# Optimization experiments

Measured on AMD Instinct MI355X. Metric: run time of the kernel, lower is better.

## Reference

```python
import jax, jax.numpy as jnp
import numpy as np

N = 50000      # nodes
E = 800000     # edges (before self-loops)
D_IN = 256     # input feature dim
H = 4          # attention heads
C = 32         # per-head channels
HID = H * C    # 128, concat output dim
BN_EPS = 1e-5


def setup_inputs() -> dict:
    key = jax.random.key(0)
    ks = jax.random.split(key, 24)
    inp = {}
    inp["x"] = jax.random.normal(ks[0], (N, D_IN), jnp.float32)
    inp["edge_index"] = jax.random.randint(ks[1], (2, E), 0, N, jnp.int32)
    # layer 1 GATConv params
    inp["W1"] = jax.random.normal(ks[2], (D_IN, HID), jnp.float32) * (2.0 / (D_IN + HID)) ** 0.5
    inp["att_src1"] = jax.random.normal(ks[3], (H, C), jnp.float32) * 0.1
    inp["att_dst1"] = jax.random.normal(ks[4], (H, C), jnp.float32) * 0.1
    inp["bias1"] = jnp.zeros((HID,), jnp.float32)
    # layer 1 BatchNorm (eval mode)
    inp["gamma1"] = 1.0 + 0.1 * jax.random.normal(ks[5], (HID,), jnp.float32)
    inp["beta1"] = 0.1 * jax.random.normal(ks[6], (HID,), jnp.float32)
    inp["mean1"] = 0.1 * jax.random.normal(ks[7], (HID,), jnp.float32)
    inp["var1"] = 0.5 + jax.random.uniform(ks[8], (HID,), jnp.float32)
    # layer 2 GATConv params
    inp["W2"] = jax.random.normal(ks[9], (HID, HID), jnp.float32) * (2.0 / (HID + HID)) ** 0.5
    inp["att_src2"] = jax.random.normal(ks[10], (H, C), jnp.float32) * 0.1
    inp["att_dst2"] = jax.random.normal(ks[11], (H, C), jnp.float32) * 0.1
    inp["bias2"] = jnp.zeros((HID,), jnp.float32)
    # layer 2 BatchNorm (eval mode)
    inp["gamma2"] = 1.0 + 0.1 * jax.random.normal(ks[12], (HID,), jnp.float32)
    inp["beta2"] = 0.1 * jax.random.normal(ks[13], (HID,), jnp.float32)
    inp["mean2"] = 0.1 * jax.random.normal(ks[14], (HID,), jnp.float32)
    inp["var2"] = 0.5 + jax.random.uniform(ks[15], (HID,), jnp.float32)
    return inp


def _gat_layer(x, src, dst, W, att_src, att_dst, bias):
    # x: [N, D]; src/dst: [Etot] with self-loops already appended
    h = (x @ W).reshape(N, H, C)                       # [N, H, C]
    a_s = jnp.einsum("nhc,hc->nh", h, att_src)         # [N, H]
    a_d = jnp.einsum("nhc,hc->nh", h, att_dst)         # [N, H]
    e = jax.nn.leaky_relu(a_s[src] + a_d[dst], 0.2)    # [Etot, H]
    # edge softmax over incoming edges of each destination node
    m = jax.ops.segment_max(e, dst, num_segments=N)    # [N, H]
    ex = jnp.exp(e - m[dst])                           # [Etot, H]
    den = jax.ops.segment_sum(ex, dst, num_segments=N) # [N, H]
    alpha = ex / (den[dst] + 1e-16)                    # [Etot, H]
    out = jax.ops.segment_sum(h[src] * alpha[:, :, None], dst, num_segments=N)
    return out.reshape(N, HID) + bias                  # concat heads + bias


def _bn_eval(x, gamma, beta, mean, var):
    return (x - mean) * (gamma * jax.lax.rsqrt(var + BN_EPS)) + beta


def reference(x, edge_index, W1, att_src1, att_dst1, bias1, gamma1, beta1, mean1, var1,
              W2, att_src2, att_dst2, bias2, gamma2, beta2, mean2, var2):
    loop = jnp.arange(N, dtype=edge_index.dtype)
    src = jnp.concatenate([edge_index[0], loop])  # PyG GATConv adds self-loops
    dst = jnp.concatenate([edge_index[1], loop])
    h = _gat_layer(x, src, dst, W1, att_src1, att_dst1, bias1)
    h = jax.nn.relu(_bn_eval(h, gamma1, beta1, mean1, var1))  # dropout = identity (eval)
    h = _gat_layer(h, src, dst, W2, att_src2, att_dst2, bias2)
    h = jax.nn.relu(_bn_eval(h, gamma2, beta2, mean2, var2))
    return h
```

## Files before the change

### kernel.cpp

```cpp
#include <hip/hip_runtime.h>
#include <math.h>

#define N_NODES 50000
#define EDGES   800000
#define ETOT    (EDGES + N_NODES)
#define HID     128
#define NH      4

typedef __attribute__((ext_vector_type(8))) short short8;
typedef __attribute__((ext_vector_type(4))) float floatx4;

__device__ inline unsigned short f2bf(float f) {
    unsigned int u = __float_as_uint(f);
    u = u + 0x7FFFu + ((u >> 16) & 1u);
    return (unsigned short)(u >> 16);
}

#define NB 391
#define BCAP 2688
#define CHUNK 4096
#define BIN_BLOCKS ((ETOT + CHUNK - 1) / CHUNK)

__global__ __launch_bounds__(256) void init_cursor_kernel(int* __restrict__ cursor) {
    int t = blockIdx.x * 256 + threadIdx.x;
    if (t < NB) cursor[t] = t * BCAP;
}

__global__ __launch_bounds__(256) void bin_scatter_kernel(const int* __restrict__ ei,
                                                          int* __restrict__ cursor,
                                                          int* __restrict__ binned) {
    __shared__ int histL[NB];
    int t = threadIdx.x;
    for (int b = t; b < NB; b += 256) histL[b] = 0;
    __syncthreads();
    int base = blockIdx.x * CHUNK;
#pragma unroll
    for (int j = 0; j < 16; j++) {
        int e = base + j * 256 + t;
        if (e < ETOT) {
            int d = (e < EDGES) ? ei[EDGES + e] : (e - EDGES);
            atomicAdd(&histL[d >> 7], 1);
        }
    }
    __syncthreads();
    for (int b = t; b < NB; b += 256) {
        int c = histL[b];
        histL[b] = c ? atomicAdd(&cursor[b], c) : 0;
    }
    __syncthreads();
#pragma unroll
    for (int j = 0; j < 16; j++) {
        int e = base + j * 256 + t;
        if (e < ETOT) {
            int s, d;
            if (e < EDGES) { s = ei[e]; d = ei[EDGES + e]; }
            else           { s = d = e - EDGES; }
            int bb = d >> 7;
            int pos = atomicAdd(&histL[bb], 1);
            if (pos < (bb + 1) * BCAP)
                binned[pos] = (s << 7) | (d & 127);
        }
    }
}

__global__ __launch_bounds__(256) void bin_finalize_kernel(const int* __restrict__ binned,
                                                           const int* __restrict__ cursor,
                                                           int* __restrict__ starts,
                                                           int* __restrict__ degs,
                                                           int* __restrict__ csr) {
    __shared__ int histN[128];
    __shared__ int excl[128];
    int b = blockIdx.x, t = threadIdx.x;
    int n0 = b << 7;
    int S = b * BCAP;
    int cnt = cursor[b] - S;
    if (cnt > BCAP) cnt = BCAP;
    if (t < 128) histN[t] = 0;
    __syncthreads();
    for (int j = t; j < cnt; j += 256)
        atomicAdd(&histN[binned[S + j] & 127], 1);
    __syncthreads();
    int v = (t < 128) ? histN[t] : 0;
    if (t < 128) excl[t] = v;
    __syncthreads();
    for (int off = 1; off < 128; off <<= 1) {
        int x = 0, add = 0;
        if (t < 128) { x = excl[t]; if (t >= off) add = excl[t - off]; }
        __syncthreads();
        if (t < 128) excl[t] = x + add;
        __syncthreads();
    }
    if (t < 128) {
        int ex = excl[t] - v;
        int n = n0 + t;
        if (n < N_NODES) { starts[n] = S + ex; degs[n] = v; }
        histN[t] = ex;
    }
    __syncthreads();
    for (int j = t; j < cnt; j += 256) {
        int e = binned[S + j];
        int pos = atomicAdd(&histN[e & 127], 1);
        csr[S + pos] = e >> 7;
    }
}

__global__ void wtrans_coef_kernel(const float* __restrict__ W1, const float* __restrict__ W2,
                                   unsigned short* __restrict__ Wt1, unsigned short* __restrict__ Wt2,
                                   const float* __restrict__ b1, const float* __restrict__ g1,
                                   const float* __restrict__ be1, const float* __restrict__ mn1,
                                   const float* __restrict__ vr1,
                                   const float* __restrict__ b2, const float* __restrict__ g2,
                                   const float* __restrict__ be2, const float* __restrict__ mn2,
                                   const float* __restrict__ vr2, float* __restrict__ coef) {
    int i = blockIdx.x * 256 + threadIdx.x;
    if (i < 256 * 128) { int k = i >> 7, n = i & 127; Wt1[n * 256 + k] = f2bf(W1[i]); }
    if (i < 128 * 128) { int k = i >> 7, n = i & 127; Wt2[n * 128 + k] = f2bf(W2[i]); }
    if (blockIdx.x == 0) {
        int t = threadIdx.x;
        if (t < 128) {
            float sc = g1[t] * rsqrtf(vr1[t] + 1e-5f);
            coef[t]       = sc;
            coef[128 + t] = be1[t] + (b1[t] - mn1[t]) * sc;
        } else {
            int c = t - 128;
            float sc = g2[c] * rsqrtf(vr2[c] + 1e-5f);
            coef[256 + c] = sc;
            coef[384 + c] = be2[c] + (b2[c] - mn2[c]) * sc;
        }
    }
}

#define GR   64
#define KC   64
#define PADK 88
#define PADH 136

union Smem {
    struct { unsigned short Xs[GR][PADK]; unsigned short Ws[HID][PADK]; } s;
    unsigned short Hs[GR][PADH];
};

template<bool XBF16>
__global__ __launch_bounds__(256) void gemm_att_kernel(const void* __restrict__ Xv,
                                                       const unsigned short* __restrict__ Wt,
                                                       const float* __restrict__ att_src,
                                                       const float* __restrict__ att_dst,
                                                       unsigned short* __restrict__ Hout,
                                                       float* __restrict__ aS,
                                                       float* __restrict__ aD, int K) {
    __shared__ Smem sm;
    int t = threadIdx.x, lane = t & 63, w = t >> 6;
    int quad = lane >> 4, nl = lane & 15;
    int rowBase = blockIdx.x * GR;

    floatx4 acc[8];
    floatx4 zero = {0.f, 0.f, 0.f, 0.f};
#pragma unroll
    for (int b = 0; b < 8; b++) acc[b] = zero;

    const float*          Xf = (const float*)Xv;
    const unsigned short* Xb = (const unsigned short*)Xv;

    for (int k0 = 0; k0 < K; k0 += KC) {
#pragma unroll
        for (int it = 0; it < 2; it++) {
            int s5 = t + it * 256;
            int row = s5 >> 3, kg = s5 & 7;
            int gr = rowBase + row;
            unsigned short tmp[8];
            if (XBF16) {
                uint4 v = make_uint4(0, 0, 0, 0);
                if (gr < N_NODES) v = *(const uint4*)&Xb[(unsigned)(gr * K + k0 + kg * 8)];
                *(uint4*)tmp = v;
            } else {
                float4 v0 = make_float4(0, 0, 0, 0), v1 = v0;
                if (gr < N_NODES) {
                    const float* p = &Xf[(unsigned)(gr * K + k0 + kg * 8)];
                    v0 = *(const float4*)p;
                    v1 = *(const float4*)(p + 4);
                }
                tmp[0] = f2bf(v0.x); tmp[1] = f2bf(v0.y); tmp[2] = f2bf(v0.z); tmp[3] = f2bf(v0.w);
                tmp[4] = f2bf(v1.x); tmp[5] = f2bf(v1.y); tmp[6] = f2bf(v1.z); tmp[7] = f2bf(v1.w);
            }
            *(uint4*)&sm.s.Xs[row][kg * 8] = *(uint4*)tmp;
        }
#pragma unroll
        for (int it = 0; it < 4; it++) {
            int s5 = t + it * 256;
            int n = s5 >> 3, kg = s5 & 7;
            *(uint4*)&sm.s.Ws[n][kg * 8] = *(const uint4*)&Wt[(unsigned)(n * K + k0 + kg * 8)];
        }
        __syncthreads();
#pragma unroll
        for (int ks = 0; ks < 2; ks++) {
            int kb = ks * 32 + quad * 8;
            short8 a0 = *(const short8*)&sm.s.Xs[w * 16 + nl][kb];
#pragma unroll
            for (int ct = 0; ct < 8; ct++) {
                short8 b = *(const short8*)&sm.s.Ws[ct * 16 + nl][kb];
                acc[ct] = __builtin_amdgcn_mfma_f32_16x16x32_bf16(a0, b, acc[ct], 0, 0, 0);
            }
        }
        __syncthreads();
    }

#pragma unroll
    for (int ct = 0; ct < 8; ct++)
#pragma unroll
        for (int r = 0; r < 4; r++)
            sm.Hs[w * 16 + quad * 4 + r][ct * 16 + nl] = f2bf(acc[ct][r]);

    float asv[8], adv[8];
    {
        const float* ap = &att_src[nl * 8];
        const float* dp = &att_dst[nl * 8];
        *(float4*)&asv[0] = *(const float4*)ap;  *(float4*)&asv[4] = *(const float4*)(ap + 4);
        *(float4*)&adv[0] = *(const float4*)dp;  *(float4*)&adv[4] = *(const float4*)(dp + 4);
    }
    int hd = nl >> 2;
#pragma unroll
    for (int it = 0; it < 4; it++) {
        int rl = w * 16 + it * 4 + quad;
        int grow = rowBase + rl;
        uint4 v = *(const uint4*)&sm.Hs[rl][nl * 8];
        float f[8];
        f[0] = __uint_as_float(v.x << 16); f[1] = __uint_as_float(v.x & 0xffff0000u);
        f[2] = __uint_as_float(v.y << 16); f[3] = __uint_as_float(v.y & 0xffff0000u);
        f[4] = __uint_as_float(v.z << 16); f[5] = __uint_as_float(v.z & 0xffff0000u);
        f[6] = __uint_as_float(v.w << 16); f[7] = __uint_as_float(v.w & 0xffff0000u);
        float ds = 0.f, dd = 0.f;
#pragma unroll
        for (int j = 0; j < 8; j++) {
            ds = fmaf(f[j], asv[j], ds);
            dd = fmaf(f[j], adv[j], dd);
        }
        ds += __shfl_xor(ds, 1); ds += __shfl_xor(ds, 2);
        dd += __shfl_xor(dd, 1); dd += __shfl_xor(dd, 2);
        if (grow < N_NODES) {
            *(uint4*)&Hout[(unsigned)(grow * HID + nl * 8)] = v;
            if ((nl & 3) == 0) { aS[grow * 4 + hd] = ds; aD[grow * 4 + hd] = dd; }
        }
    }
}

#define ECAP 64
#define ASTRIDE 65

template<bool OUTBF16>
__global__ __launch_bounds__(256) void gather_kernel(const unsigned short* __restrict__ hfeat,
                                                     const float* __restrict__ a_s,
                                                     const float* __restrict__ a_d,
                                                     const int* __restrict__ starts,
                                                     const int* __restrict__ degs,
                                                     const int* __restrict__ csr,
                                                     const float* __restrict__ coefA,
                                                     const float* __restrict__ coefB,
                                                     void* __restrict__ outv) {
    __shared__ float alphaT[4][4][ASTRIDE];
    __shared__ int   offS[4][ECAP];
    int t = threadIdx.x, lane = t & 63, ws = t >> 6;
    int h = lane >> 4, l16 = lane & 15;
    int n = blockIdx.x * 4 + ws;
    int start = starts[n];
    int deg = degs[n];
    float adh = a_d[(unsigned)(n * 4 + h)];

    float e[4];
    int   sreg[4];
#pragma unroll
    for (int it = 0; it < 4; it++) {
        int j = l16 + it * 16;
        e[it] = -1e30f;
        if (j < deg) {
            int s = csr[start + j];
            sreg[it] = s;
            float as = a_s[(unsigned)(s * 4 + h)];
            float v = as + adh;
            e[it] = v > 0.f ? v : 0.2f * v;
        }
    }
    float m = fmaxf(fmaxf(e[0], e[1]), fmaxf(e[2], e[3]));
    for (int j = ECAP + l16; j < deg; j += 16) {
        int s = csr[start + j];
        float as = a_s[(unsigned)(s * 4 + h)];
        float v = as + adh; v = v > 0.f ? v : 0.2f * v;
        m = fmaxf(m, v);
    }
#pragma unroll
    for (int off = 1; off < 16; off <<= 1) m = fmaxf(m, __shfl_xor(m, off));

    float x[4];
    float d = 0.f;
#pragma unroll
    for (int it = 0; it < 4; it++) { x[it] = __expf(e[it] - m); d += x[it]; }
    for (int j = ECAP + l16; j < deg; j += 16) {
        int s = csr[start + j];
        float as = a_s[(unsigned)(s * 4 + h)];
        float v = as + adh; v = v > 0.f ? v : 0.2f * v;
        d += __expf(v - m);
    }
#pragma unroll
    for (int off = 1; off < 16; off <<= 1) d += __shfl_xor(d, off);
    float rd = 1.0f / (d + 1e-16f);

#pragma unroll
    for (int it = 0; it < 4; it++) {
        int j = l16 + it * 16;
        if (j < deg) {
            alphaT[ws][h][j] = x[it] * rd;
            if (h == 0) offS[ws][j] = sreg[it] << 8;
        }
    }
    __syncthreads();

    int c = lane * 2;
    int lane4 = lane * 4;
    const char* hbase = (const char*)hfeat;

    float acc0 = 0.f, acc1 = 0.f;
    int cap = deg < ECAP ? deg : ECAP;
    int j = 0;
    for (; j + 7 < cap; j += 8) {
        unsigned o[8]; float a[8]; unsigned v[8];
#pragma unroll
        for (int u = 0; u < 8; u++) o[u] = (unsigned)(offS[ws][j + u] + lane4);
#pragma unroll
        for (int u = 0; u < 8; u++) a[u] = alphaT[ws][h][j + u];
#pragma unroll
        for (int u = 0; u < 8; u++) v[u] = *(const unsigned int*)(hbase + o[u]);
#pragma unroll
        for (int u = 0; u < 8; u++) {
            acc0 = fmaf(__uint_as_float(v[u] << 16),         a[u], acc0);
            acc1 = fmaf(__uint_as_float(v[u] & 0xffff0000u), a[u], acc1);
        }
    }
    for (; j < cap; j++) {
        unsigned o = (unsigned)(offS[ws][j] + lane4);
        float al = alphaT[ws][h][j];
        unsigned int v = *(const unsigned int*)(hbase + o);
        acc0 = fmaf(__uint_as_float(v << 16),         al, acc0);
        acc1 = fmaf(__uint_as_float(v & 0xffff0000u), al, acc1);
    }
    for (; j < deg; j++) {
        int s = csr[start + j];
        float as = a_s[(unsigned)(s * 4 + h)];
        float v2 = as + adh; v2 = v2 > 0.f ? v2 : 0.2f * v2;
        float al = __expf(v2 - m) * rd;
        unsigned int v = *(const unsigned int*)(hbase + (unsigned)((s << 8) + lane4));
        acc0 = fmaf(__uint_as_float(v << 16),         al, acc0);
        acc1 = fmaf(__uint_as_float(v & 0xffff0000u), al, acc1);
    }
    float2 cA = *(const float2*)&coefA[c];
    float2 cB = *(const float2*)&coefB[c];
    float o0 = fmaxf(fmaf(acc0, cA.x, cB.x), 0.f);
    float o1 = fmaxf(fmaf(acc1, cA.y, cB.y), 0.f);
    if (OUTBF16) {
        unsigned int pk = (unsigned int)f2bf(o0) | ((unsigned int)f2bf(o1) << 16);
        ((unsigned int*)outv)[(unsigned)(n * 64 + lane)] = pk;
    } else {
        ((float2*)outv)[(unsigned)(n * 64 + lane)] = make_float2(o0, o1);
    }
}

extern "C" void kernel_launch(void* const* d_in, const int* in_sizes, int n_in,
                              void* d_out, int out_size, void* d_ws, size_t ws_size,
                              hipStream_t stream) {
    const float* x    = (const float*)d_in[0];
    const int*   ei   = (const int*)d_in[1];
    const float* W1   = (const float*)d_in[2];
    const float* as1  = (const float*)d_in[3];
    const float* ad1  = (const float*)d_in[4];
    const float* b1   = (const float*)d_in[5];
    const float* g1   = (const float*)d_in[6];
    const float* be1  = (const float*)d_in[7];
    const float* mn1  = (const float*)d_in[8];
    const float* vr1  = (const float*)d_in[9];
    const float* W2   = (const float*)d_in[10];
    const float* as2  = (const float*)d_in[11];
    const float* ad2  = (const float*)d_in[12];
    const float* b2   = (const float*)d_in[13];
    const float* g2   = (const float*)d_in[14];
    const float* be2  = (const float*)d_in[15];
    const float* mn2  = (const float*)d_in[16];
    const float* vr2  = (const float*)d_in[17];
    float* out = (float*)d_out;

    unsigned short* hb  = (unsigned short*)d_ws;
    unsigned short* x2b = hb + (size_t)N_NODES * HID;
    unsigned short* Wt1 = x2b + (size_t)N_NODES * HID;
    unsigned short* Wt2 = Wt1 + 128 * 256;
    float* aS    = (float*)(Wt2 + 128 * 128);
    float* aD    = aS + N_NODES * NH;
    float* coef  = aD + N_NODES * NH;
    int* cursor  = (int*)(coef + 512);
    int* starts  = cursor + NB;
    int* degs    = starts + N_NODES;
    int* binned  = degs + N_NODES;
    int* csr     = binned + NB * BCAP;

    init_cursor_kernel<<<2, 256, 0, stream>>>(cursor);
    bin_scatter_kernel<<<BIN_BLOCKS, 256, 0, stream>>>(ei, cursor, binned);
    bin_finalize_kernel<<<NB, 256, 0, stream>>>(binned, cursor, starts, degs, csr);
    wtrans_coef_kernel<<<128, 256, 0, stream>>>(W1, W2, Wt1, Wt2,
                                                b1, g1, be1, mn1, vr1,
                                                b2, g2, be2, mn2, vr2, coef);

    int gemmGrid = (N_NODES + GR - 1) / GR;
    int nodeGrid = N_NODES / 4;

    gemm_att_kernel<false><<<gemmGrid, 256, 0, stream>>>(x, Wt1, as1, ad1, hb, aS, aD, 256);
    gather_kernel<true><<<nodeGrid, 256, 0, stream>>>(hb, aS, aD, starts, degs, csr,
                                                      coef, coef + 128, (void*)x2b);
    gemm_att_kernel<true><<<gemmGrid, 256, 0, stream>>>(x2b, Wt2, as2, ad2, hb, aS, aD, 128);
    gather_kernel<false><<<nodeGrid, 256, 0, stream>>>(hb, aS, aD, starts, degs, csr,
                                                       coef + 256, coef + 384, (void*)out);
}
```

Baseline: 262.3 us.

## Prefetch neighbor features in registers and broadcast alphas via cross-lane ops

The gather kernel no longer stages source offsets and attention weights in shared memory behind a block-wide barrier. Source indices are broadcast with readlane, and the first 16–32 neighbor feature loads are issued before the softmax max/sum reductions, so their memory latency overlaps that math. Alphas are fetched per head with ds_bpermute, using a double-buffered 16-edge register scheme. In exchange it uses more registers and always issues 16 loads per group, reading node 0 for padding slots whose weight is zero.

Result: no change. 261.2 us (-0.4%).

```diff
diff --git a/kernel.cpp b/kernel.cpp
--- a/kernel.cpp
+++ b/kernel.cpp
@@ -244,7 +244,27 @@
 }
 
 #define ECAP 64
-#define ASTRIDE 65
+
+__device__ __forceinline__ void prefetch16(unsigned (&buf)[16], int srcreg,
+                                           const char* hbase, int lane4) {
+#pragma unroll
+    for (int u = 0; u < 16; u++) {
+        int s = __builtin_amdgcn_readlane(srcreg, u);
+        buf[u] = *(const unsigned int*)(hbase + (((long)s) << 8) + lane4);
+    }
+}
+
+__device__ __forceinline__ void consume16(const unsigned (&buf)[16], float xr,
+                                          int abase, float& acc0, float& acc1) {
+#pragma unroll
+    for (int u = 0; u < 16; u++) {
+        float au = __uint_as_float((unsigned)__builtin_amdgcn_ds_bpermute(
+                        abase | (u << 2), (int)__float_as_uint(xr)));
+        unsigned vv = buf[u];
+        acc0 = fmaf(__uint_as_float(vv << 16),         au, acc0);
+        acc1 = fmaf(__uint_as_float(vv & 0xffff0000u), au, acc1);
+    }
+}
 
 template<bool OUTBF16>
 __global__ __launch_bounds__(256) void gather_kernel(const unsigned short* __restrict__ hfeat,
@@ -256,29 +276,39 @@
                                                      const float* __restrict__ coefA,
                                                      const float* __restrict__ coefB,
                                                      void* __restrict__ outv) {
-    __shared__ float alphaT[4][4][ASTRIDE];
-    __shared__ int   offS[4][ECAP];
     int t = threadIdx.x, lane = t & 63, ws = t >> 6;
     int h = lane >> 4, l16 = lane & 15;
     int n = blockIdx.x * 4 + ws;
     int start = starts[n];
     int deg = degs[n];
     float adh = a_d[(unsigned)(n * 4 + h)];
-
+    int lane4 = lane << 2;
+    int abase = (lane & 48) << 2;
+    const char* hbase = (const char*)hfeat;
+
+    int sreg[4];
+#pragma unroll
+    for (int it = 0; it < 4; it++) {
+        int j = l16 + it * 16;
+        sreg[it] = (j < deg) ? csr[start + j] : 0;
+    }
     float e[4];
-    int   sreg[4];
 #pragma unroll
     for (int it = 0; it < 4; it++) {
         int j = l16 + it * 16;
         e[it] = -1e30f;
         if (j < deg) {
-            int s = csr[start + j];
-            sreg[it] = s;
-            float as = a_s[(unsigned)(s * 4 + h)];
+            float as = a_s[(unsigned)(sreg[it] * 4 + h)];
             float v = as + adh;
             e[it] = v > 0.f ? v : 0.2f * v;
         }
     }
+
+    int cap = deg < ECAP ? deg : ECAP;
+    unsigned vA[16], vB[16];
+    prefetch16(vA, sreg[0], hbase, lane4);
+    if (cap > 16) prefetch16(vB, sreg[1], hbase, lane4);
+
     float m = fmaxf(fmaxf(e[0], e[1]), fmaxf(e[2], e[3]));
     for (int j = ECAP + l16; j < deg; j += 16) {
         int s = csr[start + j];
@@ -302,46 +332,22 @@
 #pragma unroll
     for (int off = 1; off < 16; off <<= 1) d += __shfl_xor(d, off);
     float rd = 1.0f / (d + 1e-16f);
-
-#pragma unroll
-    for (int it = 0; it < 4; it++) {
-        int j = l16 + it * 16;
-        if (j < deg) {
-            alphaT[ws][h][j] = x[it] * rd;
-            if (h == 0) offS[ws][j] = sreg[it] << 8;
-        }
-    }
-    __syncthreads();
-
-    int c = lane * 2;
-    int lane4 = lane * 4;
-    const char* hbase = (const char*)hfeat;
+    float xr[4];
+#pragma unroll
+    for (int it = 0; it < 4; it++) xr[it] = x[it] * rd;
 
     float acc0 = 0.f, acc1 = 0.f;
-    int cap = deg < ECAP ? deg : ECAP;
-    int j = 0;
-    for (; j + 7 < cap; j += 8) {
-        unsigned o[8]; float a[8]; unsigned v[8];
-#pragma unroll
-        for (int u = 0; u < 8; u++) o[u] = (unsigned)(offS[ws][j + u] + lane4);
-#pragma unroll
-        for (int u = 0; u < 8; u++) a[u] = alphaT[ws][h][j + u];
-#pragma unroll
-        for (int u = 0; u < 8; u++) v[u] = *(const unsigned int*)(hbase + o[u]);
-#pragma unroll
-        for (int u = 0; u < 8; u++) {
-            acc0 = fmaf(__uint_as_float(v[u] << 16),         a[u], acc0);
-            acc1 = fmaf(__uint_as_float(v[u] & 0xffff0000u), a[u], acc1);
-        }
-    }
-    for (; j < cap; j++) {
-        unsigned o = (unsigned)(offS[ws][j] + lane4);
-        float al = alphaT[ws][h][j];
-        unsigned int v = *(const unsigned int*)(hbase + o);
-        acc0 = fmaf(__uint_as_float(v << 16),         al, acc0);
-        acc1 = fmaf(__uint_as_float(v & 0xffff0000u), al, acc1);
-    }
-    for (; j < deg; j++) {
+    consume16(vA, xr[0], abase, acc0, acc1);
+    if (cap > 16) {
+        if (cap > 32) prefetch16(vA, sreg[2], hbase, lane4);
+        consume16(vB, xr[1], abase, acc0, acc1);
+        if (cap > 32) {
+            if (cap > 48) prefetch16(vB, sreg[3], hbase, lane4);
+            consume16(vA, xr[2], abase, acc0, acc1);
+            if (cap > 48) consume16(vB, xr[3], abase, acc0, acc1);
+        }
+    }
+    for (int j = ECAP; j < deg; j++) {
         int s = csr[start + j];
         float as = a_s[(unsigned)(s * 4 + h)];
         float v2 = as + adh; v2 = v2 > 0.f ? v2 : 0.2f * v2;
@@ -350,6 +356,8 @@
         acc0 = fmaf(__uint_as_float(v << 16),         al, acc0);
         acc1 = fmaf(__uint_as_float(v & 0xffff0000u), al, acc1);
     }
+
+    int c = lane * 2;
     float2 cA = *(const float2*)&coefA[c];
     float2 cB = *(const float2*)&coefB[c];
     float o0 = fmaxf(fmaf(acc0, cA.x, cB.x), 0.f);
```
